# Kernel optimization log

Hardware: AMD Instinct MI355X
Metric: run time of the kernel (lower is better)

The kernel has to match this reference:

```python
import jax, jax.numpy as jnp
import numpy as np

B, L, DIM = 8, 512, 8          # batch, seq len, raw channels (value dim D = 2*DIM = 16)
ET, HID, H = 128, 128, 2       # embed_time, hidden_size, num_heads
MAXLEN = 512
NEG = -1e9


def setup_inputs() -> dict:
    key = jax.random.key(0)
    ks = jax.random.split(key, 40)
    def n(i, shape, s=0.05):
        return jax.random.normal(ks[i], shape, jnp.float32) * s
    vals = jax.random.normal(ks[0], (B, L, DIM), jnp.float32)
    msk = (jax.random.uniform(ks[1], (B, L, DIM)) > 0.2).astype(jnp.float32)
    x = jnp.concatenate([vals, msk], -1)                      # (B, L, 2*DIM)
    time_steps = jax.random.uniform(ks[2], (B, L), jnp.float32)
    return {
        'x': x, 'time_steps': time_steps,
        # learned time embedding: Linear(1, ET-1) periodic + Linear(1,1)
        'w_per': n(3, (1, ET - 1)), 'b_per': n(4, (ET - 1,)),
        'w_lin': n(5, (1, 1)), 'b_lin': n(6, (1,)),
        # MultiTimeAttention projections
        'Wq_t': n(7, (ET, ET)), 'bq_t': n(8, (ET,)),
        'Wk_t': n(9, (ET, ET)), 'bk_t': n(10, (ET,)),
        'Wo_t': n(11, (2 * DIM * H, HID)), 'bo_t': n(12, (HID,)),
        'pos_emb': n(13, (MAXLEN + 1, HID)), 'cls_emb': n(14, (1, HID)),
        # transformer block (BERT-style post-LN encoder layer, d_ff=HID)
        'tWq': n(15, (HID, HID)), 'tbq': n(16, (HID,)),
        'tWk': n(17, (HID, HID)), 'tbk': n(18, (HID,)),
        'tWv': n(19, (HID, HID)), 'tbv': n(20, (HID,)),
        'tWo': n(21, (HID, HID)), 'tbo': n(22, (HID,)),
        'ln1_g': jnp.ones((HID,), jnp.float32), 'ln1_b': jnp.zeros((HID,), jnp.float32),
        'fW1': n(23, (HID, HID)), 'fb1': n(24, (HID,)),
        'fW2': n(25, (HID, HID)), 'fb2': n(26, (HID,)),
        'ln2_g': jnp.ones((HID,), jnp.float32), 'ln2_b': jnp.zeros((HID,), jnp.float32),
        # BertPooler
        'pW': n(27, (HID, HID)), 'pb': n(28, (HID,)),
    }


def _time_emb(tt, w_per, b_per, w_lin, b_lin):
    tt = tt[..., None]                                        # (B, L, 1)
    return jnp.concatenate([tt @ w_lin + b_lin, jnp.sin(tt @ w_per + b_per)], -1)


def _ln(x, g, b, eps=1e-5):
    m = x.mean(-1, keepdims=True)
    v = ((x - m) ** 2).mean(-1, keepdims=True)
    return (x - m) / jnp.sqrt(v + eps) * g + b


def _mta(q_emb, k_emb, value, mask, Wq, bq, Wk, bk, Wo, bo):
    # MultiTimeAttention: scores broadcast to value-channel axis, softmax over keys
    D = value.shape[-1]
    dk = ET // H
    def split(e, W, b):
        p = e @ W + b
        return p.reshape(e.shape[0], -1, H, dk).transpose(0, 2, 1, 3)
    q = split(q_emb, Wq, bq)                                  # (Bq, H, Lq, dk)
    k = split(k_emb, Wk, bk)                                  # (B,  H, Lk, dk)
    scores = jnp.matmul(q, k.swapaxes(-1, -2)) / jnp.sqrt(jnp.float32(dk))  # (B,H,Lq,Lk)
    s5 = jnp.where(mask[:, None, None, :, :] == 0, NEG, scores[..., None])  # (B,H,Lq,Lk,D)
    p = jax.nn.softmax(s5, axis=-2)
    out = jnp.einsum('bhqkd,bkd->bhqd', p, value)             # (B, H, Lq, D)
    Bv = value.shape[0]
    out = out.transpose(0, 2, 1, 3).reshape(Bv, -1, H * D)
    return out @ Wo + bo


def _tblock(x, tWq, tbq, tWk, tbk, tWv, tbv, tWo, tbo, ln1_g, ln1_b,
            fW1, fb1, fW2, fb2, ln2_g, ln2_b):
    Bq, Lq, _ = x.shape
    dk = HID // H
    def heads(W, b):
        return (x @ W + b).reshape(Bq, Lq, H, dk).transpose(0, 2, 1, 3)
    q, k, v = heads(tWq, tbq), heads(tWk, tbk), heads(tWv, tbv)
    a = jax.nn.softmax(jnp.matmul(q, k.swapaxes(-1, -2)) / jnp.sqrt(jnp.float32(dk)), -1)
    o = jnp.matmul(a, v).transpose(0, 2, 1, 3).reshape(Bq, Lq, HID) @ tWo + tbo
    x = _ln(x + o, ln1_g, ln1_b)
    f = jax.nn.relu(x @ fW1 + fb1) @ fW2 + fb2
    return _ln(x + f, ln2_g, ln2_b)


def reference(x, time_steps, w_per, b_per, w_lin, b_lin,
              Wq_t, bq_t, Wk_t, bk_t, Wo_t, bo_t, pos_emb, cls_emb,
              tWq, tbq, tWk, tbk, tWv, tbv, tWo, tbo, ln1_g, ln1_b,
              fW1, fb1, fW2, fb2, ln2_g, ln2_b, pW, pb):
    Bx = x.shape[0]
    mask_half = x[:, :, DIM:]
    mask = jnp.concatenate([mask_half, mask_half], -1)        # (B, L, 2*DIM)
    key_e = _time_emb(time_steps, w_per, b_per, w_lin, b_lin)
    tq_e = _time_emb(time_steps, w_per, b_per, w_lin, b_lin)  # query_time_steps=None -> same
    cls_t = jnp.linspace(0.0, 1.0, 128, dtype=jnp.float32)[None]
    cls_q_e = _time_emb(cls_t, w_per, b_per, w_lin, b_lin)    # (1, 128, ET)
    cls_out = _mta(cls_q_e, key_e, x, mask, Wq_t, bq_t, Wk_t, bk_t, Wo_t, bo_t)
    out = _mta(tq_e, key_e, x, mask, Wq_t, bq_t, Wk_t, bk_t, Wo_t, bo_t)
    tb = (tWq, tbq, tWk, tbk, tWv, tbv, tWo, tbo, ln1_g, ln1_b,
          fW1, fb1, fW2, fb2, ln2_g, ln2_b)
    cls_repr = jnp.broadcast_to(cls_emb[None, :, :], (Bx, 1, HID))
    # encode(cls_out, is_pooling=True), pooling='bert': no pos emb, take token 0
    h = _tblock(jnp.concatenate([cls_repr, cls_out], 1), *tb)
    cls_pooling = jnp.tanh(h[:, 0] @ pW + pb)                 # (B, HID)
    # encode(out, is_pooling=False) [pretrain path]: pos emb + transformer, drop CLS
    h2 = jnp.concatenate([cls_repr, out], 1)                  # (B, L+1, HID)
    h2 = h2 + pos_emb[:h2.shape[1]][None]
    h2 = _tblock(h2, *tb)
    last_hidden_state = h2[:, 1:]                             # (B, L, HID)
    return cls_pooling, last_hidden_state
```

## Files before the change

### kernel.cpp

```cpp
#include <hip/hip_runtime.h>
#include <hip/hip_bf16.h>
#include <math.h>


static constexpr int NM_ = 8 * 513;
static constexpr int NC_ = 8 * 129;
static constexpr int NT_ = NM_ + NC_;
static constexpr int VTS_ = 5248;

using bf = __hip_bfloat16;
typedef __attribute__((ext_vector_type(8))) short bf16x8;
typedef __attribute__((ext_vector_type(4))) short bf16x4;
typedef __attribute__((ext_vector_type(4))) float floatx4;
typedef __attribute__((ext_vector_type(8))) unsigned short ushortx8;

__device__ __forceinline__ float wave_reduce_sum(float v) {
    #pragma unroll
    for (int off = 32; off >= 1; off >>= 1) v += __shfl_xor(v, off);
    return v;
}
__device__ __forceinline__ float wave_reduce_max(float v) {
    #pragma unroll
    for (int off = 32; off >= 1; off >>= 1) v = fmaxf(v, __shfl_xor(v, off));
    return v;
}
__device__ __forceinline__ float u2f(unsigned short u) {
    return __uint_as_float(((unsigned)u) << 16);
}
__device__ __forceinline__ unsigned short f2u(float f) {
    unsigned u = __float_as_uint(f);
    return (unsigned short)((u + 0x7FFF + ((u >> 16) & 1)) >> 16);
}
__device__ __forceinline__ bf16x8 join8(bf16x4 lo, bf16x4 hi) {
    return __builtin_shufflevector(lo, hi, 0, 1, 2, 3, 4, 5, 6, 7);
}
__device__ __forceinline__ float rdin(const void* p, int i, int flag) {
    return flag ? u2f(((const unsigned short*)p)[i]) : ((const float*)p)[i];
}

struct PrepAll {
    const void* src[32]; int n[32]; int dstoff[32];
    int cstart[32]; int cnum[32];
    int ncv;
    const void* wsrc[8]; unsigned short* wdst[8]; float wscale[8];
    const void* ts; const void* w_per; const void* b_per;
    const void* w_lin; const void* b_lin;
    unsigned short* key_e16;
    unsigned short* btg;
    const void* xsrc;
    unsigned short* vt;
    const unsigned short* det;
};
__global__ void prep_all_kernel(PrepAll a, float* dst) {
    int flag = (a.det[0] == 0x3F80u) ? 1 : 0;
    int blk = blockIdx.x, tid = threadIdx.x;
    if (blk < a.ncv) {
        int which = -1, bi = 0;
        #pragma unroll
        for (int i = 0; i < 32; ++i)
            if (blk >= a.cstart[i] && blk < a.cstart[i] + a.cnum[i]) { which = i; bi = blk - a.cstart[i]; }
        if (which < 0) return;
        int i = bi * 256 + tid;
        if (i < a.n[which]) dst[a.dstoff[which] + i] = rdin(a.src[which], i, flag);
    } else if (blk < a.ncv + 512) {
        int p = blk - a.ncv;
        int m = p >> 6;
        int idx = (p & 63) * 256 + tid;
        int c = idx >> 9;
        int l = (idx >> 3) & 63;
        int j = idx & 7;
        int k = (c >> 3) * 32 + (l >> 4) * 8 + j;
        int n = (c & 7) * 16 + (l & 15);
        a.wdst[m][idx] = f2u(rdin(a.wsrc[m], k * 128 + n, flag) * a.wscale[m]);
    } else if (blk < a.ncv + 512 + 2112) {
        int p = blk - a.ncv - 512;
        int row = p * 2 + (tid >> 7), j = tid & 127;
        float t = (row < 4096) ? rdin(a.ts, row, flag)
                               : (float)(row - 4096) * (1.0f / 127.0f);
        float v;
        if (j == 0) v = t * rdin(a.w_lin, 0, flag) + rdin(a.b_lin, 0, flag);
        else        v = sinf(t * rdin(a.w_per, j - 1, flag) + rdin(a.b_per, j - 1, flag));
        a.key_e16[row * 128 + j] = f2u(v);
    } else if (blk < a.ncv + 512 + 2112 + 32) {
        int p = blk - a.ncv - 512 - 2112;
        int e0 = (p * 256 + tid) * 8;
        int b = e0 >> 13;
        int c = (e0 >> 9) & 15;
        int k0 = e0 & 511;
        unsigned short out[8];
        #pragma unroll
        for (int j = 0; j < 8; ++j) {
            int k = k0 + j;
            float m = rdin(a.xsrc, (b * 512 + k) * 16 + 8 + (c & 7), flag);
            float val = (c < 8) ? rdin(a.xsrc, (b * 512 + k) * 16 + c, flag) * m : m;
            out[j] = f2u(val);
        }
        *(ushortx8*)(a.btg + e0) = *(ushortx8*)out;
    } else {
        int p = blk - a.ncv - 512 - 2112 - 32;
        int idx = p * 256 + tid;
        int n = idx / 14, c8 = idx - n * 14;
        ushortx8 z = {0, 0, 0, 0, 0, 0, 0, 0};
        *(ushortx8*)(a.vt + (size_t)n * VTS_ + 5136 + c8 * 8) = z;
    }
}

struct GemmM {
    const void* A[3]; const unsigned short* W[3]; const float* bias[3];
    unsigned short* C[3];
    int M[3]; float bscale[3];
};
__global__ void __launch_bounds__(256)
gemm_mfma_kernel(GemmM p) {
    int y = blockIdx.y;
    const unsigned short* Wsw = p.W[y];
    const float* bias = p.bias[y];
    unsigned short* C = p.C[y];
    int M = p.M[y];
    float bscale = p.bscale[y];
    int m0 = blockIdx.x * 16;
    if (m0 >= M) return;
    int tid = threadIdx.x;
    int wv = tid >> 6, lane = tid & 63;
    int am = lane & 15, aq = lane >> 4;
    const unsigned short* A = (const unsigned short*)p.A[y];
    const unsigned short* Arow = A + (size_t)(m0 + am) * 128;
    floatx4 acc0 = {0.f, 0.f, 0.f, 0.f}, acc1 = acc0;
    #pragma unroll
    for (int ks = 0; ks < 4; ++ks) {
        bf16x8 af = *(const bf16x8*)(Arow + ks * 32 + aq * 8);
        const unsigned short* base = Wsw + ((size_t)ks * 8 + 2 * wv) * 512 + lane * 8;
        bf16x8 b0 = *(const bf16x8*)(base);
        bf16x8 b1 = *(const bf16x8*)(base + 512);
        acc0 = __builtin_amdgcn_mfma_f32_16x16x32_bf16(af, b0, acc0, 0, 0, 0);
        acc1 = __builtin_amdgcn_mfma_f32_16x16x32_bf16(af, b1, acc1, 0, 0, 0);
    }
    int col = lane & 15, rowb = (lane >> 4) * 4;
    #pragma unroll
    for (int t = 0; t < 2; ++t) {
        floatx4 acc = t ? acc1 : acc0;
        int n = wv * 32 + t * 16 + col;
        float bv = bias[n] * bscale;
        #pragma unroll
        for (int rg = 0; rg < 4; ++rg)
            C[(size_t)(m0 + rowb + rg) * 128 + n] = f2u(acc[rg] + bv);
    }
}

__global__ void __launch_bounds__(256)
mta_att_kernel(const unsigned short* qp_cls, const unsigned short* qp_main,
               const unsigned short* kp, const unsigned short* btg,
               float* att_cls, float* att_mn) {
    int is_cls = (blockIdx.x >= 32);
    int qt = is_cls ? (blockIdx.x - 32) : blockIdx.x;
    int h = blockIdx.y, b = blockIdx.z;
    int tid = threadIdx.x, lane = tid & 63, wv = tid >> 6;
    __shared__ unsigned short sp[16][520];
    __shared__ float red[1024 + 256];
    int q0 = qt * 16;
    int m = lane & 15, g = lane >> 4;

    const unsigned short* qrow = is_cls ? (qp_cls + (size_t)(q0 + m) * 128 + h * 64)
                                        : (qp_main + (size_t)(b * 512 + q0 + m) * 128 + h * 64);
    bf16x8 qf0 = *(const bf16x8*)(qrow + g * 8);
    bf16x8 qf1 = *(const bf16x8*)(qrow + 32 + g * 8);

    const unsigned short* kbase = kp + ((size_t)b * 512) * 128 + h * 64;
    #pragma unroll
    for (int kt = 0; kt < 8; ++kt) {
        int colk = kt * 64 + wv * 16 + m;
        const unsigned short* kb = kbase + (size_t)colk * 128;
        bf16x8 b0 = *(const bf16x8*)(kb + g * 8);
        bf16x8 b1 = *(const bf16x8*)(kb + 32 + g * 8);
        floatx4 acc = {0.f, 0.f, 0.f, 0.f};
        acc = __builtin_amdgcn_mfma_f32_16x16x32_bf16(qf0, b0, acc, 0, 0, 0);
        acc = __builtin_amdgcn_mfma_f32_16x16x32_bf16(qf1, b1, acc, 0, 0, 0);
        #pragma unroll
        for (int rg = 0; rg < 4; ++rg) sp[g * 4 + rg][colk] = f2u(acc[rg]);
    }
    __syncthreads();

    for (int rr = wv; rr < 16; rr += 4) {
        float mx = -1e30f;
        for (int k = lane; k < 512; k += 64) mx = fmaxf(mx, u2f(sp[rr][k]));
        mx = wave_reduce_max(mx);
        for (int k = lane; k < 512; k += 64) sp[rr][k] = f2u(expf(u2f(sp[rr][k]) - mx));
    }
    __syncthreads();

    floatx4 macc = {0.f, 0.f, 0.f, 0.f};
    {
        const unsigned short* bbase = btg + ((size_t)(b * 16 + m)) * 512 + g * 8;
        #pragma unroll
        for (int cc = 0; cc < 4; ++cc) {
            int koff = (wv + cc * 4) * 32;
            bf16x8 af = *(const bf16x8*)&sp[m][koff + g * 8];
            bf16x8 bfv = *(const bf16x8*)(bbase + koff);
            macc = __builtin_amdgcn_mfma_f32_16x16x32_bf16(af, bfv, macc, 0, 0, 0);
        }
    }
    float* redC = red;
    float* Cfull = red + 1024;
    #pragma unroll
    for (int rg = 0; rg < 4; ++rg) redC[tid * 4 + rg] = macc[rg];
    __syncthreads();
    {
        int l = tid >> 2, rg = tid & 3;
        float s = redC[l * 4 + rg] + redC[(64 + l) * 4 + rg]
                + redC[(128 + l) * 4 + rg] + redC[(192 + l) * 4 + rg];
        int row = (l >> 4) * 4 + rg, c = l & 15;
        Cfull[row * 16 + c] = s;
    }
    __syncthreads();
    if (tid < 128) {
        int r = tid >> 3, c = tid & 7;
        float num = Cfull[r * 16 + c];
        float den = Cfull[r * 16 + 8 + c];
        int row = q0 + r;
        float* dst = is_cls ? (att_cls + (size_t)(b * 128 + row) * 32)
                            : (att_mn + (size_t)(b * 512 + row) * 32);
        dst[h * 16 + c] = num / den;
        dst[h * 16 + 8 + c] = 1.0f;
    }
}

__global__ void __launch_bounds__(256)
mta_qkv_kernel(const float* att, const float* Wo, const float* bo,
               const float* cls_emb, const float* pos, float* xin,
               const unsigned short* Wq, const unsigned short* Wk, const unsigned short* Wv,
               const float* bq, const float* bk, const float* bv_,
               unsigned short* outq, unsigned short* outk, unsigned short* vT) {
    int m0 = blockIdx.x * 16;
    __shared__ float As32[16][36];
    __shared__ unsigned short As[16][136];
    int tid = threadIdx.x;
    int r = tid >> 4, g = tid & 15, c0 = g * 8;

    int R = m0 + r;
    int srow, prow;
    if (R < NM_) {
        int b = R / 513, rr = R - b * 513;
        srow = (rr == 0) ? -1 : 1024 + b * 512 + (rr - 1);
        prow = rr;
    } else {
        int mc = R - NM_;
        int b = mc / 129, rr = mc - b * 129;
        srow = (rr == 0) ? -1 : b * 128 + (rr - 1);
        prow = -1;
    }
    if (g < 2 && srow >= 0) {
        const float* src = att + (size_t)srow * 32 + g * 16;
        *(float4*)&As32[r][g * 16]      = *(const float4*)(src);
        *(float4*)&As32[r][g * 16 + 4]  = *(const float4*)(src + 4);
        *(float4*)&As32[r][g * 16 + 8]  = *(const float4*)(src + 8);
        *(float4*)&As32[r][g * 16 + 12] = *(const float4*)(src + 12);
    }
    __syncthreads();

    float acc[8];
    if (srow < 0) {
        #pragma unroll
        for (int j = 0; j < 8; ++j) acc[j] = cls_emb[c0 + j];
    } else {
        #pragma unroll
        for (int j = 0; j < 8; ++j) acc[j] = bo[c0 + j];
        #pragma unroll 8
        for (int k = 0; k < 32; ++k) {
            float a = As32[r][k];
            const float4 w0 = *(const float4*)(Wo + (size_t)k * 128 + c0);
            const float4 w1 = *(const float4*)(Wo + (size_t)k * 128 + c0 + 4);
            acc[0] = fmaf(a, w0.x, acc[0]); acc[1] = fmaf(a, w0.y, acc[1]);
            acc[2] = fmaf(a, w0.z, acc[2]); acc[3] = fmaf(a, w0.w, acc[3]);
            acc[4] = fmaf(a, w1.x, acc[4]); acc[5] = fmaf(a, w1.y, acc[5]);
            acc[6] = fmaf(a, w1.z, acc[6]); acc[7] = fmaf(a, w1.w, acc[7]);
        }
    }
    if (prow >= 0) {
        const float* pr = pos + (size_t)prow * 128 + c0;
        float4 p0 = *(const float4*)(pr);
        float4 p1 = *(const float4*)(pr + 4);
        acc[0] += p0.x; acc[1] += p0.y; acc[2] += p0.z; acc[3] += p0.w;
        acc[4] += p1.x; acc[5] += p1.y; acc[6] += p1.z; acc[7] += p1.w;
    }
    *(float4*)(xin + (size_t)R * 128 + c0) = make_float4(acc[0], acc[1], acc[2], acc[3]);
    *(float4*)(xin + (size_t)R * 128 + c0 + 4) = make_float4(acc[4], acc[5], acc[6], acc[7]);
    *(ushort4*)&As[r][c0] = make_ushort4(f2u(acc[0]), f2u(acc[1]), f2u(acc[2]), f2u(acc[3]));
    *(ushort4*)&As[r][c0 + 4] = make_ushort4(f2u(acc[4]), f2u(acc[5]), f2u(acc[6]), f2u(acc[7]));
    __syncthreads();

    int wv = tid >> 6, lane = tid & 63;
    int am = lane & 15, aq = lane >> 4;
    int col = lane & 15, rowb = (lane >> 4) * 4;
    const unsigned short* Ws[3] = {Wq, Wk, Wv};
    const float* bs[3] = {bq, bk, bv_};
    float bsc[3] = {0.125f, 1.f, 1.f};
    unsigned short* Cs[2] = {outq, outk};
    #pragma unroll
    for (int y = 0; y < 3; ++y) {
        floatx4 acc0 = {0.f, 0.f, 0.f, 0.f}, acc1 = acc0;
        #pragma unroll
        for (int ks = 0; ks < 4; ++ks) {
            bf16x8 af = *(bf16x8*)&As[am][ks * 32 + aq * 8];
            const unsigned short* base = Ws[y] + ((size_t)ks * 8 + 2 * wv) * 512 + lane * 8;
            bf16x8 b0 = *(const bf16x8*)(base);
            bf16x8 b1 = *(const bf16x8*)(base + 512);
            acc0 = __builtin_amdgcn_mfma_f32_16x16x32_bf16(af, b0, acc0, 0, 0, 0);
            acc1 = __builtin_amdgcn_mfma_f32_16x16x32_bf16(af, b1, acc1, 0, 0, 0);
        }
        #pragma unroll
        for (int t = 0; t < 2; ++t) {
            floatx4 a2 = t ? acc1 : acc0;
            int n = wv * 32 + t * 16 + col;
            float bvv = bs[y][n] * bsc[y];
            #pragma unroll
            for (int rg = 0; rg < 4; ++rg) {
                unsigned short val = f2u(a2[rg] + bvv);
                if (y < 2) Cs[y][(size_t)(m0 + rowb + rg) * 128 + n] = val;
                else       vT[(size_t)n * VTS_ + (m0 + rowb + rg)] = val;
            }
        }
    }
}

__global__ void __launch_bounds__(256)
tb_att_kernel(const unsigned short* qp, const unsigned short* kp,
              const unsigned short* vT, unsigned short* outp) {
    int is_cls = (blockIdx.x >= 33);
    int qt = is_cls ? blockIdx.x - 33 : blockIdx.x;
    int h = blockIdx.y, b = blockIdx.z;
    int Lq = is_cls ? 129 : 513;
    int base = is_cls ? (4104 + b * 129) : (b * 513);
    int nkt = is_cls ? 3 : 9;
    int tid = threadIdx.x, lane = tid & 63, wv = tid >> 6;
    __shared__ unsigned short sp[16][588];
    __shared__ float rinv[16];
    int q0 = qt * 16;
    int m = lane & 15, g = lane >> 4;

    int qr = q0 + m; if (qr >= Lq) qr = Lq - 1;
    const unsigned short* qrow = qp + (size_t)(base + qr) * 128 + h * 64;
    bf16x8 qf0 = *(const bf16x8*)(qrow + g * 8);
    bf16x8 qf1 = *(const bf16x8*)(qrow + 32 + g * 8);

    for (int kt = 0; kt < nkt; ++kt) {
        int colk = kt * 64 + wv * 16 + m;
        int krow = (colk < Lq) ? colk : (Lq - 1);
        const unsigned short* kb = kp + (size_t)(base + krow) * 128 + h * 64;
        bf16x8 b0 = *(const bf16x8*)(kb + g * 8);
        bf16x8 b1 = *(const bf16x8*)(kb + 32 + g * 8);
        floatx4 acc = {0.f, 0.f, 0.f, 0.f};
        acc = __builtin_amdgcn_mfma_f32_16x16x32_bf16(qf0, b0, acc, 0, 0, 0);
        acc = __builtin_amdgcn_mfma_f32_16x16x32_bf16(qf1, b1, acc, 0, 0, 0);
        #pragma unroll
        for (int rg = 0; rg < 4; ++rg)
            sp[g * 4 + rg][colk] = f2u((colk < Lq) ? acc[rg] : -1e30f);
    }
    __syncthreads();

    int kend = nkt * 64;
    for (int rr = wv; rr < 16; rr += 4) {
        float mx = -1e30f;
        for (int k = lane; k < kend; k += 64) mx = fmaxf(mx, u2f(sp[rr][k]));
        mx = wave_reduce_max(mx);
        float sum = 0.f;
        for (int k = lane; k < kend; k += 64) {
            float e = expf(u2f(sp[rr][k]) - mx);
            sp[rr][k] = f2u(e);
            sum += e;
        }
        sum = wave_reduce_sum(sum);
        if (lane == 0) rinv[rr] = 1.f / sum;
    }
    __syncthreads();

    floatx4 oacc = {0.f, 0.f, 0.f, 0.f};
    const unsigned short* vbase = vT + (size_t)(h * 64 + wv * 16 + m) * VTS_ + base;
    for (int kt = 0; kt < nkt; ++kt) {
        int k0 = kt * 64;
        #pragma unroll
        for (int c = 0; c < 2; ++c) {
            bf16x4 plo = *(const bf16x4*)&sp[m][k0 + c * 32 + g * 8];
            bf16x4 phi = *(const bf16x4*)&sp[m][k0 + c * 32 + g * 8 + 4];
            bf16x8 vf = *(const bf16x8*)(vbase + k0 + c * 32 + g * 8);
            oacc = __builtin_amdgcn_mfma_f32_16x16x32_bf16(join8(plo, phi), vf, oacc, 0, 0, 0);
        }
    }
    int dcol = wv * 16 + m;
    #pragma unroll
    for (int rg = 0; rg < 4; ++rg) {
        int q = g * 4 + rg;
        int qout = q0 + q;
        if (qout < Lq)
            outp[(size_t)(base + qout) * 128 + h * 64 + dcol] = f2u(oacc[rg] * rinv[q]);
    }
}

__global__ void __launch_bounds__(256)
attnout_ffn_kernel(const unsigned short* A, const unsigned short* Wao, const float* bao,
                   const float* resid, const float* g1, const float* b1ln,
                   const unsigned short* W1, const float* fb1,
                   const unsigned short* W2, const float* fb2,
                   const float* g2, const float* b2ln,
                   const float* pW, const float* pb, float* dout) {
    int m0 = blockIdx.x * 16;
    __shared__ unsigned short As[16][136];
    __shared__ float Xs[16][128];
    __shared__ unsigned short Hs[16][136];
    __shared__ float redS[4][4][4], redQ[4][4][4];
    __shared__ float smean[16], sinv[16];
    __shared__ float x2row[128];
    __shared__ int poolb;
    int tid = threadIdx.x;
    if (tid == 0) poolb = -1;
    {
        int r = tid >> 4, c0 = (tid & 15) * 8;
        *(ushortx8*)&As[r][c0] = *(const ushortx8*)(A + (size_t)(m0 + r) * 128 + c0);
    }
    __syncthreads();

    int wv = tid >> 6, lane = tid & 63;
    int am = lane & 15, aq = lane >> 4;
    int col = lane & 15, g = lane >> 4, rowb = g * 4;

    float ov[2][4];
    {
        floatx4 acc0 = {0.f, 0.f, 0.f, 0.f}, acc1 = acc0;
        #pragma unroll
        for (int ks = 0; ks < 4; ++ks) {
            bf16x8 af = *(bf16x8*)&As[am][ks * 32 + aq * 8];
            const unsigned short* base = Wao + ((size_t)ks * 8 + 2 * wv) * 512 + lane * 8;
            bf16x8 bb0 = *(const bf16x8*)(base);
            bf16x8 bb1 = *(const bf16x8*)(base + 512);
            acc0 = __builtin_amdgcn_mfma_f32_16x16x32_bf16(af, bb0, acc0, 0, 0, 0);
            acc1 = __builtin_amdgcn_mfma_f32_16x16x32_bf16(af, bb1, acc1, 0, 0, 0);
        }
        #pragma unroll
        for (int t = 0; t < 2; ++t) {
            int n = wv * 32 + t * 16 + col;
            float bv = bao[n];
            floatx4 acc = t ? acc1 : acc0;
            #pragma unroll
            for (int rg = 0; rg < 4; ++rg)
                ov[t][rg] = acc[rg] + bv + resid[(size_t)(m0 + rowb + rg) * 128 + n];
        }
    }
    #pragma unroll
    for (int rg = 0; rg < 4; ++rg) {
        float s = ov[0][rg] + ov[1][rg];
        float q = ov[0][rg] * ov[0][rg] + ov[1][rg] * ov[1][rg];
        #pragma unroll
        for (int off = 8; off >= 1; off >>= 1) {
            s += __shfl_xor(s, off);
            q += __shfl_xor(q, off);
        }
        if ((lane & 15) == 0) { redS[wv][g][rg] = s; redQ[wv][g][rg] = q; }
    }
    __syncthreads();
    if (tid < 16) {
        int gg = tid >> 2, rg = tid & 3;
        float s = redS[0][gg][rg] + redS[1][gg][rg] + redS[2][gg][rg] + redS[3][gg][rg];
        float q = redQ[0][gg][rg] + redQ[1][gg][rg] + redQ[2][gg][rg] + redQ[3][gg][rg];
        float mean = s * 0.0078125f;
        float var = q * 0.0078125f - mean * mean;
        smean[tid] = mean;
        sinv[tid] = rsqrtf(var + 1e-5f);
    }
    __syncthreads();
    #pragma unroll
    for (int t = 0; t < 2; ++t) {
        int n = wv * 32 + t * 16 + col;
        float gm = g1[n], bb = b1ln[n];
        #pragma unroll
        for (int rg = 0; rg < 4; ++rg) {
            int row = rowb + rg;
            float val = (ov[t][rg] - smean[row]) * sinv[row] * gm + bb;
            Xs[row][n] = val;
            As[row][n] = f2u(val);
        }
    }
    __syncthreads();

    {
        floatx4 acc0 = {0.f, 0.f, 0.f, 0.f}, acc1 = acc0;
        #pragma unroll
        for (int ks = 0; ks < 4; ++ks) {
            bf16x8 af = *(bf16x8*)&As[am][ks * 32 + aq * 8];
            const unsigned short* base = W1 + ((size_t)ks * 8 + 2 * wv) * 512 + lane * 8;
            bf16x8 bb0 = *(const bf16x8*)(base);
            bf16x8 bb1 = *(const bf16x8*)(base + 512);
            acc0 = __builtin_amdgcn_mfma_f32_16x16x32_bf16(af, bb0, acc0, 0, 0, 0);
            acc1 = __builtin_amdgcn_mfma_f32_16x16x32_bf16(af, bb1, acc1, 0, 0, 0);
        }
        #pragma unroll
        for (int t = 0; t < 2; ++t) {
            int n = wv * 32 + t * 16 + col;
            float bv = fb1[n];
            floatx4 acc = t ? acc1 : acc0;
            #pragma unroll
            for (int rg = 0; rg < 4; ++rg)
                Hs[rowb + rg][n] = f2u(fmaxf(acc[rg] + bv, 0.f));
        }
    }
    __syncthreads();

    floatx4 acc0 = {0.f, 0.f, 0.f, 0.f}, acc1 = acc0;
    #pragma unroll
    for (int ks = 0; ks < 4; ++ks) {
        bf16x8 af = *(bf16x8*)&Hs[am][ks * 32 + aq * 8];
        const unsigned short* base = W2 + ((size_t)ks * 8 + 2 * wv) * 512 + lane * 8;
        bf16x8 bb0 = *(const bf16x8*)(base);
        bf16x8 bb1 = *(const bf16x8*)(base + 512);
        acc0 = __builtin_amdgcn_mfma_f32_16x16x32_bf16(af, bb0, acc0, 0, 0, 0);
        acc1 = __builtin_amdgcn_mfma_f32_16x16x32_bf16(af, bb1, acc1, 0, 0, 0);
    }
    #pragma unroll
    for (int t = 0; t < 2; ++t) {
        int n = wv * 32 + t * 16 + col;
        float bv = fb2[n];
        floatx4 acc = t ? acc1 : acc0;
        #pragma unroll
        for (int rg = 0; rg < 4; ++rg)
            ov[t][rg] = acc[rg] + bv + Xs[rowb + rg][n];
    }
    #pragma unroll
    for (int rg = 0; rg < 4; ++rg) {
        float s = ov[0][rg] + ov[1][rg];
        float q = ov[0][rg] * ov[0][rg] + ov[1][rg] * ov[1][rg];
        #pragma unroll
        for (int off = 8; off >= 1; off >>= 1) {
            s += __shfl_xor(s, off);
            q += __shfl_xor(q, off);
        }
        if ((lane & 15) == 0) { redS[wv][g][rg] = s; redQ[wv][g][rg] = q; }
    }
    __syncthreads();
    if (tid < 16) {
        int gg = tid >> 2, rg = tid & 3;
        float s = redS[0][gg][rg] + redS[1][gg][rg] + redS[2][gg][rg] + redS[3][gg][rg];
        float q = redQ[0][gg][rg] + redQ[1][gg][rg] + redQ[2][gg][rg] + redQ[3][gg][rg];
        float mean = s * 0.0078125f;
        float var = q * 0.0078125f - mean * mean;
        smean[tid] = mean;
        sinv[tid] = rsqrtf(var + 1e-5f);
    }
    __syncthreads();
    #pragma unroll
    for (int t = 0; t < 2; ++t) {
        int n = wv * 32 + t * 16 + col;
        float gm = g2[n], bb = b2ln[n];
        #pragma unroll
        for (int rg = 0; rg < 4; ++rg) {
            int row = rowb + rg;
            int m = m0 + row;
            float val = (ov[t][rg] - smean[row]) * sinv[row] * gm + bb;
            if (m < NM_) {
                int b = m / 513, r = m - b * 513;
                if (r >= 1)
                    dout[1024 + (size_t)b * 65536 + (size_t)(r - 1) * 128 + n] = val;
            } else {
                int mc = m - NM_;
                int b = mc / 129, r = mc - b * 129;
                if (r == 0) {
                    x2row[n] = val;
                    if (n == 0) poolb = b;
                }
            }
        }
    }
    __syncthreads();
    if (poolb >= 0 && tid < 128) {
        float acc = pb[tid];
        for (int k = 0; k < 128; ++k) acc = fmaf(x2row[k], pW[(size_t)k * 128 + tid], acc);
        dout[(size_t)poolb * 128 + tid] = tanhf(acc);
    }
}

extern "C" void kernel_launch(void* const* d_in, const int* in_sizes, int n_in,
                              void* d_out, int out_size, void* d_ws, size_t ws_size,
                              hipStream_t stream) {
    float* w = (float*)d_ws;
    size_t off = 0;
    auto alloc = [&](size_t n) {
        float* p = w + off;
        off += (n + 3) & ~(size_t)3;
        return p;
    };
    auto allocU = [&](size_t n) { return (unsigned short*)alloc((n + 1) / 2); };

    PrepAll pa{};
    int nn = n_in < 32 ? n_in : 32;
    float* fin[32];
    const int needconv[32] = {0,0,0,0,0,0, 0,1, 0,1, 1,1, 1,1, 0,1, 0,1, 0,1,
                              0,1, 1,1, 0,1, 0,1, 1,1, 1,1};
    int ncv = 0;
    for (int i = 0; i < nn; ++i) {
        pa.src[i] = d_in[i];
        pa.n[i] = in_sizes[i];
        fin[i] = alloc(in_sizes[i]);
        pa.dstoff[i] = (int)(fin[i] - w);
        if (needconv[i]) {
            int nb = (in_sizes[i] + 255) / 256;
            pa.cstart[i] = ncv;
            pa.cnum[i] = nb;
            ncv += nb;
        } else { pa.cstart[i] = -1; pa.cnum[i] = 0; }
    }
    for (int i = nn; i < 32; ++i) {
        pa.src[i] = nullptr; pa.n[i] = 0; pa.dstoff[i] = 0;
        pa.cstart[i] = -1; pa.cnum[i] = 0;
    }
    pa.ncv = ncv;

    const float* bq_t    = fin[7];
    const float* bk_t    = fin[9];
    const float* Wo_t    = fin[10]; const float* bo_t = fin[11];
    const float* pos_emb = fin[12]; const float* cls_emb = fin[13];
    const float* tbq = fin[15]; const float* tbk = fin[17]; const float* tbv = fin[19];
    const float* tbo = fin[21];
    const float* ln1_g = fin[22]; const float* ln1_b = fin[23];
    const float* fb1 = fin[25]; const float* fb2 = fin[27];
    const float* ln2_g = fin[28]; const float* ln2_b = fin[29];
    const float* pW = fin[30]; const float* pb = fin[31];

    const int widx[8] = {8, 6, 14, 16, 18, 20, 24, 26};
    unsigned short* wsw[8];
    for (int i = 0; i < 8; ++i) {
        wsw[i] = allocU(16384);
        pa.wsrc[i] = d_in[widx[i]];
        pa.wdst[i] = wsw[i];
        pa.wscale[i] = (i == 1 || i == 2) ? 0.125f : 1.0f;
    }
    pa.ts = d_in[1]; pa.w_per = d_in[2]; pa.b_per = d_in[3];
    pa.w_lin = d_in[4]; pa.b_lin = d_in[5];
    pa.xsrc = d_in[0];
    pa.det = (const unsigned short*)d_in[22];

    unsigned short* key_e16 = allocU(4224 * 128);
    unsigned short* cls_e16 = key_e16 + 4096 * 128;
    pa.key_e16 = key_e16;
    unsigned short* btg = allocU(8 * 16 * 512);
    pa.btg = btg;

    unsigned short* qp_main16 = allocU(4096 * 128);
    unsigned short* kp_main16 = allocU(4096 * 128);
    unsigned short* qp_cls16  = allocU(128 * 128);
    float* att_all = alloc(5120 * 32);
    float* att_cls = att_all;
    float* att_mn  = att_all + 1024 * 32;
    float* xin     = alloc((size_t)NT_ * 128);
    unsigned short* tbq16 = allocU((size_t)NT_ * 128);
    unsigned short* tbk16 = allocU((size_t)NT_ * 128);
    unsigned short* vT    = allocU((size_t)128 * VTS_);
    unsigned short* tba16 = allocU((size_t)NT_ * 128);
    pa.vt = vT;
    (void)ws_size;

    float* outf = (float*)d_out;

    prep_all_kernel<<<ncv + 512 + 2112 + 32 + 7, 256, 0, stream>>>(pa, w);

    {
        GemmM p{};
        p.A[0] = key_e16; p.W[0] = wsw[0]; p.bias[0] = bk_t; p.C[0] = kp_main16;
        p.M[0] = 4096; p.bscale[0] = 1.f;
        p.A[1] = key_e16; p.W[1] = wsw[1]; p.bias[1] = bq_t; p.C[1] = qp_main16;
        p.M[1] = 4096; p.bscale[1] = 0.125f;
        p.A[2] = cls_e16; p.W[2] = wsw[1]; p.bias[2] = bq_t; p.C[2] = qp_cls16;
        p.M[2] = 128; p.bscale[2] = 0.125f;
        gemm_mfma_kernel<<<dim3(256, 3), 256, 0, stream>>>(p);
    }

    mta_att_kernel<<<dim3(40, 2, 8), 256, 0, stream>>>(qp_cls16, qp_main16, kp_main16,
                                                       btg, att_cls, att_mn);

    mta_qkv_kernel<<<321, 256, 0, stream>>>(att_all, Wo_t, bo_t, cls_emb, pos_emb, xin,
                                            wsw[2], wsw[3], wsw[4], tbq, tbk, tbv,
                                            tbq16, tbk16, vT);

    tb_att_kernel<<<dim3(42, 2, 8), 256, 0, stream>>>(tbq16, tbk16, vT, tba16);

    attnout_ffn_kernel<<<321, 256, 0, stream>>>(tba16, wsw[5], tbo, xin, ln1_g, ln1_b,
                                                wsw[6], fb1, wsw[7], fb2, ln2_g, ln2_b,
                                                pW, pb, outf);
}
```

Before: 188.2 us.

## Fuse all pipeline stages into one cooperative persistent kernel with grid syncs

Replaces the six separate kernel launches with a single cooperative kernel that runs every stage as a grid-stride loop over virtual blocks, separated by grid-wide barriers, with shared memory held in a union across stages. Each stage body is pulled out into a device function so the old multi-launch path stays as a fallback when cooperative launch is unavailable. The aim is to remove per-launch overhead and the idle gaps between short kernels. In exchange it adds grid-barrier cost, caps the grid at what fits resident, and pays host-side occupancy and attribute queries on every call.

After: 429.6 us. +128.3%, slower.

```diff
diff --git a/kernel.cpp b/kernel.cpp
--- a/kernel.cpp
+++ b/kernel.cpp
@@ -1,6 +1,9 @@
 #include <hip/hip_runtime.h>
 #include <hip/hip_bf16.h>
+#include <hip/hip_cooperative_groups.h>
 #include <math.h>
+
+namespace cg = cooperative_groups;
 
 
 static constexpr int NM_ = 8 * 513;
@@ -37,6 +40,16 @@
 __device__ __forceinline__ float rdin(const void* p, int i, int flag) {
     return flag ? u2f(((const unsigned short*)p)[i]) : ((const float*)p)[i];
 }
+
+struct MaS { unsigned short sp[16][520]; float red[1280]; };
+struct MqS { float As32[16][36]; unsigned short As[16][136]; };
+struct TbS { unsigned short sp[16][588]; float rinv[16]; };
+struct AoS {
+    unsigned short As[16][136]; float Xs[16][128]; unsigned short Hs[16][136];
+    float redS[4][4][4], redQ[4][4][4], smean[16], sinv[16], x2row[128];
+    int poolb;
+};
+union SMem { MaS ma; MqS mq; TbS tb; AoS ao; };
 
 struct PrepAll {
     const void* src[32]; int n[32]; int dstoff[32];
@@ -51,17 +64,18 @@
     unsigned short* vt;
     const unsigned short* det;
 };
-__global__ void prep_all_kernel(PrepAll a, float* dst) {
-    int flag = (a.det[0] == 0x3F80u) ? 1 : 0;
-    int blk = blockIdx.x, tid = threadIdx.x;
+
+__device__ __forceinline__ void prep_body(const PrepAll& a, float* dst, int blk,
+                                          int tid, int flag) {
     if (blk < a.ncv) {
         int which = -1, bi = 0;
         #pragma unroll
         for (int i = 0; i < 32; ++i)
             if (blk >= a.cstart[i] && blk < a.cstart[i] + a.cnum[i]) { which = i; bi = blk - a.cstart[i]; }
-        if (which < 0) return;
-        int i = bi * 256 + tid;
-        if (i < a.n[which]) dst[a.dstoff[which] + i] = rdin(a.src[which], i, flag);
+        if (which >= 0) {
+            int i = bi * 256 + tid;
+            if (i < a.n[which]) dst[a.dstoff[which] + i] = rdin(a.src[which], i, flag);
+        }
     } else if (blk < a.ncv + 512) {
         int p = blk - a.ncv;
         int m = p >> 6;
@@ -99,10 +113,17 @@
     } else {
         int p = blk - a.ncv - 512 - 2112 - 32;
         int idx = p * 256 + tid;
-        int n = idx / 14, c8 = idx - n * 14;
-        ushortx8 z = {0, 0, 0, 0, 0, 0, 0, 0};
-        *(ushortx8*)(a.vt + (size_t)n * VTS_ + 5136 + c8 * 8) = z;
-    }
+        if (idx < 128 * 14) {
+            int n = idx / 14, c8 = idx - n * 14;
+            ushortx8 z = {0, 0, 0, 0, 0, 0, 0, 0};
+            *(ushortx8*)(a.vt + (size_t)n * VTS_ + 5136 + c8 * 8) = z;
+        }
+    }
+}
+
+__global__ void prep_all_kernel(PrepAll a, float* dst) {
+    int flag = (a.det[0] == 0x3F80u) ? 1 : 0;
+    prep_body(a, dst, blockIdx.x, threadIdx.x, flag);
 }
 
 struct GemmM {
@@ -110,20 +131,12 @@
     unsigned short* C[3];
     int M[3]; float bscale[3];
 };
-__global__ void __launch_bounds__(256)
-gemm_mfma_kernel(GemmM p) {
-    int y = blockIdx.y;
-    const unsigned short* Wsw = p.W[y];
-    const float* bias = p.bias[y];
-    unsigned short* C = p.C[y];
-    int M = p.M[y];
-    float bscale = p.bscale[y];
-    int m0 = blockIdx.x * 16;
-    if (m0 >= M) return;
-    int tid = threadIdx.x;
+
+__device__ __forceinline__ void gemm_body(const unsigned short* A, const unsigned short* Wsw,
+                                          const float* bias, unsigned short* C,
+                                          float bscale, int m0, int tid) {
     int wv = tid >> 6, lane = tid & 63;
     int am = lane & 15, aq = lane >> 4;
-    const unsigned short* A = (const unsigned short*)p.A[y];
     const unsigned short* Arow = A + (size_t)(m0 + am) * 128;
     floatx4 acc0 = {0.f, 0.f, 0.f, 0.f}, acc1 = acc0;
     #pragma unroll
@@ -148,15 +161,22 @@
 }
 
 __global__ void __launch_bounds__(256)
-mta_att_kernel(const unsigned short* qp_cls, const unsigned short* qp_main,
-               const unsigned short* kp, const unsigned short* btg,
-               float* att_cls, float* att_mn) {
-    int is_cls = (blockIdx.x >= 32);
-    int qt = is_cls ? (blockIdx.x - 32) : blockIdx.x;
-    int h = blockIdx.y, b = blockIdx.z;
-    int tid = threadIdx.x, lane = tid & 63, wv = tid >> 6;
-    __shared__ unsigned short sp[16][520];
-    __shared__ float red[1024 + 256];
+gemm_mfma_kernel(GemmM p) {
+    int y = blockIdx.y;
+    int m0 = blockIdx.x * 16;
+    if (m0 >= p.M[y]) return;
+    gemm_body((const unsigned short*)p.A[y], p.W[y], p.bias[y], p.C[y], p.bscale[y],
+              m0, threadIdx.x);
+}
+
+__device__ __forceinline__ void mta_att_body(
+    const unsigned short* qp_cls, const unsigned short* qp_main,
+    const unsigned short* kp, const unsigned short* btg,
+    float* att_cls, float* att_mn,
+    int is_cls, int qt, int h, int b, int tid, MaS* S)
+{
+    __syncthreads();
+    int lane = tid & 63, wv = tid >> 6;
     int q0 = qt * 16;
     int m = lane & 15, g = lane >> 4;
 
@@ -176,15 +196,15 @@
         acc = __builtin_amdgcn_mfma_f32_16x16x32_bf16(qf0, b0, acc, 0, 0, 0);
         acc = __builtin_amdgcn_mfma_f32_16x16x32_bf16(qf1, b1, acc, 0, 0, 0);
         #pragma unroll
-        for (int rg = 0; rg < 4; ++rg) sp[g * 4 + rg][colk] = f2u(acc[rg]);
+        for (int rg = 0; rg < 4; ++rg) S->sp[g * 4 + rg][colk] = f2u(acc[rg]);
     }
     __syncthreads();
 
     for (int rr = wv; rr < 16; rr += 4) {
         float mx = -1e30f;
-        for (int k = lane; k < 512; k += 64) mx = fmaxf(mx, u2f(sp[rr][k]));
+        for (int k = lane; k < 512; k += 64) mx = fmaxf(mx, u2f(S->sp[rr][k]));
         mx = wave_reduce_max(mx);
-        for (int k = lane; k < 512; k += 64) sp[rr][k] = f2u(expf(u2f(sp[rr][k]) - mx));
+        for (int k = lane; k < 512; k += 64) S->sp[rr][k] = f2u(expf(u2f(S->sp[rr][k]) - mx));
     }
     __syncthreads();
 
@@ -194,13 +214,13 @@
         #pragma unroll
         for (int cc = 0; cc < 4; ++cc) {
             int koff = (wv + cc * 4) * 32;
-            bf16x8 af = *(const bf16x8*)&sp[m][koff + g * 8];
+            bf16x8 af = *(const bf16x8*)&S->sp[m][koff + g * 8];
             bf16x8 bfv = *(const bf16x8*)(bbase + koff);
             macc = __builtin_amdgcn_mfma_f32_16x16x32_bf16(af, bfv, macc, 0, 0, 0);
         }
     }
-    float* redC = red;
-    float* Cfull = red + 1024;
+    float* redC = S->red;
+    float* Cfull = S->red + 1024;
     #pragma unroll
     for (int rg = 0; rg < 4; ++rg) redC[tid * 4 + rg] = macc[rg];
     __syncthreads();
@@ -225,15 +245,25 @@
 }
 
 __global__ void __launch_bounds__(256)
-mta_qkv_kernel(const float* att, const float* Wo, const float* bo,
-               const float* cls_emb, const float* pos, float* xin,
-               const unsigned short* Wq, const unsigned short* Wk, const unsigned short* Wv,
-               const float* bq, const float* bk, const float* bv_,
-               unsigned short* outq, unsigned short* outk, unsigned short* vT) {
-    int m0 = blockIdx.x * 16;
-    __shared__ float As32[16][36];
-    __shared__ unsigned short As[16][136];
-    int tid = threadIdx.x;
+mta_att_kernel(const unsigned short* qp_cls, const unsigned short* qp_main,
+               const unsigned short* kp, const unsigned short* btg,
+               float* att_cls, float* att_mn) {
+    __shared__ MaS S;
+    int xx = blockIdx.x;
+    mta_att_body(qp_cls, qp_main, kp, btg, att_cls, att_mn,
+                 xx >= 32, (xx >= 32) ? xx - 32 : xx, blockIdx.y, blockIdx.z,
+                 threadIdx.x, &S);
+}
+
+__device__ __forceinline__ void mta_qkv_body(
+    const float* att, const float* Wo, const float* bo,
+    const float* cls_emb, const float* pos, float* xin,
+    const unsigned short* Wq, const unsigned short* Wk, const unsigned short* Wv,
+    const float* bq, const float* bk, const float* bv_,
+    unsigned short* outq, unsigned short* outk, unsigned short* vT,
+    int m0, int tid, MqS* S)
+{
+    __syncthreads();
     int r = tid >> 4, g = tid & 15, c0 = g * 8;
 
     int R = m0 + r;
@@ -250,10 +280,10 @@
     }
     if (g < 2 && srow >= 0) {
         const float* src = att + (size_t)srow * 32 + g * 16;
-        *(float4*)&As32[r][g * 16]      = *(const float4*)(src);
-        *(float4*)&As32[r][g * 16 + 4]  = *(const float4*)(src + 4);
-        *(float4*)&As32[r][g * 16 + 8]  = *(const float4*)(src + 8);
-        *(float4*)&As32[r][g * 16 + 12] = *(const float4*)(src + 12);
+        *(float4*)&S->As32[r][g * 16]      = *(const float4*)(src);
+        *(float4*)&S->As32[r][g * 16 + 4]  = *(const float4*)(src + 4);
+        *(float4*)&S->As32[r][g * 16 + 8]  = *(const float4*)(src + 8);
+        *(float4*)&S->As32[r][g * 16 + 12] = *(const float4*)(src + 12);
     }
     __syncthreads();
 
@@ -266,7 +296,7 @@
         for (int j = 0; j < 8; ++j) acc[j] = bo[c0 + j];
         #pragma unroll 8
         for (int k = 0; k < 32; ++k) {
-            float a = As32[r][k];
+            float a = S->As32[r][k];
             const float4 w0 = *(const float4*)(Wo + (size_t)k * 128 + c0);
             const float4 w1 = *(const float4*)(Wo + (size_t)k * 128 + c0 + 4);
             acc[0] = fmaf(a, w0.x, acc[0]); acc[1] = fmaf(a, w0.y, acc[1]);
@@ -284,8 +314,8 @@
     }
     *(float4*)(xin + (size_t)R * 128 + c0) = make_float4(acc[0], acc[1], acc[2], acc[3]);
     *(float4*)(xin + (size_t)R * 128 + c0 + 4) = make_float4(acc[4], acc[5], acc[6], acc[7]);
-    *(ushort4*)&As[r][c0] = make_ushort4(f2u(acc[0]), f2u(acc[1]), f2u(acc[2]), f2u(acc[3]));
-    *(ushort4*)&As[r][c0 + 4] = make_ushort4(f2u(acc[4]), f2u(acc[5]), f2u(acc[6]), f2u(acc[7]));
+    *(ushort4*)&S->As[r][c0] = make_ushort4(f2u(acc[0]), f2u(acc[1]), f2u(acc[2]), f2u(acc[3]));
+    *(ushort4*)&S->As[r][c0 + 4] = make_ushort4(f2u(acc[4]), f2u(acc[5]), f2u(acc[6]), f2u(acc[7]));
     __syncthreads();
 
     int wv = tid >> 6, lane = tid & 63;
@@ -300,7 +330,7 @@
         floatx4 acc0 = {0.f, 0.f, 0.f, 0.f}, acc1 = acc0;
         #pragma unroll
         for (int ks = 0; ks < 4; ++ks) {
-            bf16x8 af = *(bf16x8*)&As[am][ks * 32 + aq * 8];
+            bf16x8 af = *(bf16x8*)&S->As[am][ks * 32 + aq * 8];
             const unsigned short* base = Ws[y] + ((size_t)ks * 8 + 2 * wv) * 512 + lane * 8;
             bf16x8 b0 = *(const bf16x8*)(base);
             bf16x8 b1 = *(const bf16x8*)(base + 512);
@@ -323,17 +353,26 @@
 }
 
 __global__ void __launch_bounds__(256)
-tb_att_kernel(const unsigned short* qp, const unsigned short* kp,
-              const unsigned short* vT, unsigned short* outp) {
-    int is_cls = (blockIdx.x >= 33);
-    int qt = is_cls ? blockIdx.x - 33 : blockIdx.x;
-    int h = blockIdx.y, b = blockIdx.z;
+mta_qkv_kernel(const float* att, const float* Wo, const float* bo,
+               const float* cls_emb, const float* pos, float* xin,
+               const unsigned short* Wq, const unsigned short* Wk, const unsigned short* Wv,
+               const float* bq, const float* bk, const float* bv_,
+               unsigned short* outq, unsigned short* outk, unsigned short* vT) {
+    __shared__ MqS S;
+    mta_qkv_body(att, Wo, bo, cls_emb, pos, xin, Wq, Wk, Wv, bq, bk, bv_,
+                 outq, outk, vT, blockIdx.x * 16, threadIdx.x, &S);
+}
+
+__device__ __forceinline__ void tb_att_body(
+    const unsigned short* qp, const unsigned short* kp,
+    const unsigned short* vT, unsigned short* outp,
+    int is_cls, int qt, int h, int b, int tid, TbS* S)
+{
+    __syncthreads();
     int Lq = is_cls ? 129 : 513;
     int base = is_cls ? (4104 + b * 129) : (b * 513);
     int nkt = is_cls ? 3 : 9;
-    int tid = threadIdx.x, lane = tid & 63, wv = tid >> 6;
-    __shared__ unsigned short sp[16][588];
-    __shared__ float rinv[16];
+    int lane = tid & 63, wv = tid >> 6;
     int q0 = qt * 16;
     int m = lane & 15, g = lane >> 4;
 
@@ -353,23 +392,23 @@
         acc = __builtin_amdgcn_mfma_f32_16x16x32_bf16(qf1, b1, acc, 0, 0, 0);
         #pragma unroll
         for (int rg = 0; rg < 4; ++rg)
-            sp[g * 4 + rg][colk] = f2u((colk < Lq) ? acc[rg] : -1e30f);
+            S->sp[g * 4 + rg][colk] = f2u((colk < Lq) ? acc[rg] : -1e30f);
     }
     __syncthreads();
 
     int kend = nkt * 64;
     for (int rr = wv; rr < 16; rr += 4) {
         float mx = -1e30f;
-        for (int k = lane; k < kend; k += 64) mx = fmaxf(mx, u2f(sp[rr][k]));
+        for (int k = lane; k < kend; k += 64) mx = fmaxf(mx, u2f(S->sp[rr][k]));
         mx = wave_reduce_max(mx);
         float sum = 0.f;
         for (int k = lane; k < kend; k += 64) {
-            float e = expf(u2f(sp[rr][k]) - mx);
-            sp[rr][k] = f2u(e);
+            float e = expf(u2f(S->sp[rr][k]) - mx);
+            S->sp[rr][k] = f2u(e);
             sum += e;
         }
         sum = wave_reduce_sum(sum);
-        if (lane == 0) rinv[rr] = 1.f / sum;
+        if (lane == 0) S->rinv[rr] = 1.f / sum;
     }
     __syncthreads();
 
@@ -379,8 +418,8 @@
         int k0 = kt * 64;
         #pragma unroll
         for (int c = 0; c < 2; ++c) {
-            bf16x4 plo = *(const bf16x4*)&sp[m][k0 + c * 32 + g * 8];
-            bf16x4 phi = *(const bf16x4*)&sp[m][k0 + c * 32 + g * 8 + 4];
+            bf16x4 plo = *(const bf16x4*)&S->sp[m][k0 + c * 32 + g * 8];
+            bf16x4 phi = *(const bf16x4*)&S->sp[m][k0 + c * 32 + g * 8 + 4];
             bf16x8 vf = *(const bf16x8*)(vbase + k0 + c * 32 + g * 8);
             oacc = __builtin_amdgcn_mfma_f32_16x16x32_bf16(join8(plo, phi), vf, oacc, 0, 0, 0);
         }
@@ -391,7 +430,190 @@
         int q = g * 4 + rg;
         int qout = q0 + q;
         if (qout < Lq)
-            outp[(size_t)(base + qout) * 128 + h * 64 + dcol] = f2u(oacc[rg] * rinv[q]);
+            outp[(size_t)(base + qout) * 128 + h * 64 + dcol] = f2u(oacc[rg] * S->rinv[q]);
+    }
+}
+
+__global__ void __launch_bounds__(256)
+tb_att_kernel(const unsigned short* qp, const unsigned short* kp,
+              const unsigned short* vT, unsigned short* outp) {
+    __shared__ TbS S;
+    int xx = blockIdx.x;
+    tb_att_body(qp, kp, vT, outp, xx >= 33, (xx >= 33) ? xx - 33 : xx,
+                blockIdx.y, blockIdx.z, threadIdx.x, &S);
+}
+
+__device__ __forceinline__ void attnout_body(
+    const unsigned short* A, const unsigned short* Wao, const float* bao,
+    const float* resid, const float* g1, const float* b1ln,
+    const unsigned short* W1, const float* fb1,
+    const unsigned short* W2, const float* fb2,
+    const float* g2, const float* b2ln,
+    const float* pW, const float* pb, float* dout,
+    int m0, int tid, AoS* S)
+{
+    __syncthreads();
+    if (tid == 0) S->poolb = -1;
+    {
+        int r = tid >> 4, c0 = (tid & 15) * 8;
+        *(ushortx8*)&S->As[r][c0] = *(const ushortx8*)(A + (size_t)(m0 + r) * 128 + c0);
+    }
+    __syncthreads();
+
+    int wv = tid >> 6, lane = tid & 63;
+    int am = lane & 15, aq = lane >> 4;
+    int col = lane & 15, g = lane >> 4, rowb = g * 4;
+
+    float ov[2][4];
+    {
+        floatx4 acc0 = {0.f, 0.f, 0.f, 0.f}, acc1 = acc0;
+        #pragma unroll
+        for (int ks = 0; ks < 4; ++ks) {
+            bf16x8 af = *(bf16x8*)&S->As[am][ks * 32 + aq * 8];
+            const unsigned short* base = Wao + ((size_t)ks * 8 + 2 * wv) * 512 + lane * 8;
+            bf16x8 bb0 = *(const bf16x8*)(base);
+            bf16x8 bb1 = *(const bf16x8*)(base + 512);
+            acc0 = __builtin_amdgcn_mfma_f32_16x16x32_bf16(af, bb0, acc0, 0, 0, 0);
+            acc1 = __builtin_amdgcn_mfma_f32_16x16x32_bf16(af, bb1, acc1, 0, 0, 0);
+        }
+        #pragma unroll
+        for (int t = 0; t < 2; ++t) {
+            int n = wv * 32 + t * 16 + col;
+            float bv = bao[n];
+            floatx4 acc = t ? acc1 : acc0;
+            #pragma unroll
+            for (int rg = 0; rg < 4; ++rg)
+                ov[t][rg] = acc[rg] + bv + resid[(size_t)(m0 + rowb + rg) * 128 + n];
+        }
+    }
+    #pragma unroll
+    for (int rg = 0; rg < 4; ++rg) {
+        float s = ov[0][rg] + ov[1][rg];
+        float q = ov[0][rg] * ov[0][rg] + ov[1][rg] * ov[1][rg];
+        #pragma unroll
+        for (int off = 8; off >= 1; off >>= 1) {
+            s += __shfl_xor(s, off);
+            q += __shfl_xor(q, off);
+        }
+        if ((lane & 15) == 0) { S->redS[wv][g][rg] = s; S->redQ[wv][g][rg] = q; }
+    }
+    __syncthreads();
+    if (tid < 16) {
+        int gg = tid >> 2, rg = tid & 3;
+        float s = S->redS[0][gg][rg] + S->redS[1][gg][rg] + S->redS[2][gg][rg] + S->redS[3][gg][rg];
+        float q = S->redQ[0][gg][rg] + S->redQ[1][gg][rg] + S->redQ[2][gg][rg] + S->redQ[3][gg][rg];
+        float mean = s * 0.0078125f;
+        float var = q * 0.0078125f - mean * mean;
+        S->smean[tid] = mean;
+        S->sinv[tid] = rsqrtf(var + 1e-5f);
+    }
+    __syncthreads();
+    #pragma unroll
+    for (int t = 0; t < 2; ++t) {
+        int n = wv * 32 + t * 16 + col;
+        float gm = g1[n], bb = b1ln[n];
+        #pragma unroll
+        for (int rg = 0; rg < 4; ++rg) {
+            int row = rowb + rg;
+            float val = (ov[t][rg] - S->smean[row]) * S->sinv[row] * gm + bb;
+            S->Xs[row][n] = val;
+            S->As[row][n] = f2u(val);
+        }
+    }
+    __syncthreads();
+
+    {
+        floatx4 acc0 = {0.f, 0.f, 0.f, 0.f}, acc1 = acc0;
+        #pragma unroll
+        for (int ks = 0; ks < 4; ++ks) {
+            bf16x8 af = *(bf16x8*)&S->As[am][ks * 32 + aq * 8];
+            const unsigned short* base = W1 + ((size_t)ks * 8 + 2 * wv) * 512 + lane * 8;
+            bf16x8 bb0 = *(const bf16x8*)(base);
+            bf16x8 bb1 = *(const bf16x8*)(base + 512);
+            acc0 = __builtin_amdgcn_mfma_f32_16x16x32_bf16(af, bb0, acc0, 0, 0, 0);
+            acc1 = __builtin_amdgcn_mfma_f32_16x16x32_bf16(af, bb1, acc1, 0, 0, 0);
+        }
+        #pragma unroll
+        for (int t = 0; t < 2; ++t) {
+            int n = wv * 32 + t * 16 + col;
+            float bv = fb1[n];
+            floatx4 acc = t ? acc1 : acc0;
+            #pragma unroll
+            for (int rg = 0; rg < 4; ++rg)
+                S->Hs[rowb + rg][n] = f2u(fmaxf(acc[rg] + bv, 0.f));
+        }
+    }
+    __syncthreads();
+
+    floatx4 acc0 = {0.f, 0.f, 0.f, 0.f}, acc1 = acc0;
+    #pragma unroll
+    for (int ks = 0; ks < 4; ++ks) {
+        bf16x8 af = *(bf16x8*)&S->Hs[am][ks * 32 + aq * 8];
+        const unsigned short* base = W2 + ((size_t)ks * 8 + 2 * wv) * 512 + lane * 8;
+        bf16x8 bb0 = *(const bf16x8*)(base);
+        bf16x8 bb1 = *(const bf16x8*)(base + 512);
+        acc0 = __builtin_amdgcn_mfma_f32_16x16x32_bf16(af, bb0, acc0, 0, 0, 0);
+        acc1 = __builtin_amdgcn_mfma_f32_16x16x32_bf16(af, bb1, acc1, 0, 0, 0);
+    }
+    #pragma unroll
+    for (int t = 0; t < 2; ++t) {
+        int n = wv * 32 + t * 16 + col;
+        float bv = fb2[n];
+        floatx4 acc = t ? acc1 : acc0;
+        #pragma unroll
+        for (int rg = 0; rg < 4; ++rg)
+            ov[t][rg] = acc[rg] + bv + S->Xs[rowb + rg][n];
+    }
+    #pragma unroll
+    for (int rg = 0; rg < 4; ++rg) {
+        float s = ov[0][rg] + ov[1][rg];
+        float q = ov[0][rg] * ov[0][rg] + ov[1][rg] * ov[1][rg];
+        #pragma unroll
+        for (int off = 8; off >= 1; off >>= 1) {
+            s += __shfl_xor(s, off);
+            q += __shfl_xor(q, off);
+        }
+        if ((lane & 15) == 0) { S->redS[wv][g][rg] = s; S->redQ[wv][g][rg] = q; }
+    }
+    __syncthreads();
+    if (tid < 16) {
+        int gg = tid >> 2, rg = tid & 3;
+        float s = S->redS[0][gg][rg] + S->redS[1][gg][rg] + S->redS[2][gg][rg] + S->redS[3][gg][rg];
+        float q = S->redQ[0][gg][rg] + S->redQ[1][gg][rg] + S->redQ[2][gg][rg] + S->redQ[3][gg][rg];
+        float mean = s * 0.0078125f;
+        float var = q * 0.0078125f - mean * mean;
+        S->smean[tid] = mean;
+        S->sinv[tid] = rsqrtf(var + 1e-5f);
+    }
+    __syncthreads();
+    #pragma unroll
+    for (int t = 0; t < 2; ++t) {
+        int n = wv * 32 + t * 16 + col;
+        float gm = g2[n], bb = b2ln[n];
+        #pragma unroll
+        for (int rg = 0; rg < 4; ++rg) {
+            int row = rowb + rg;
+            int mm = m0 + row;
+            float val = (ov[t][rg] - S->smean[row]) * S->sinv[row] * gm + bb;
+            if (mm < NM_) {
+                int b = mm / 513, r = mm - b * 513;
+                if (r >= 1)
+                    dout[1024 + (size_t)b * 65536 + (size_t)(r - 1) * 128 + n] = val;
+            } else {
+                int mc = mm - NM_;
+                int b = mc / 129, r = mc - b * 129;
+                if (r == 0) {
+                    S->x2row[n] = val;
+                    if (n == 0) S->poolb = b;
+                }
+            }
+        }
+    }
+    __syncthreads();
+    if (S->poolb >= 0 && tid < 128) {
+        float acc = pb[tid];
+        for (int k = 0; k < 128; ++k) acc = fmaf(S->x2row[k], pW[(size_t)k * 128 + tid], acc);
+        dout[(size_t)S->poolb * 128 + tid] = tanhf(acc);
     }
 }
 
@@ -402,177 +624,73 @@
                    const unsigned short* W2, const float* fb2,
                    const float* g2, const float* b2ln,
                    const float* pW, const float* pb, float* dout) {
-    int m0 = blockIdx.x * 16;
-    __shared__ unsigned short As[16][136];
-    __shared__ float Xs[16][128];
-    __shared__ unsigned short Hs[16][136];
-    __shared__ float redS[4][4][4], redQ[4][4][4];
-    __shared__ float smean[16], sinv[16];
-    __shared__ float x2row[128];
-    __shared__ int poolb;
+    __shared__ AoS S;
+    attnout_body(A, Wao, bao, resid, g1, b1ln, W1, fb1, W2, fb2, g2, b2ln,
+                 pW, pb, dout, blockIdx.x * 16, threadIdx.x, &S);
+}
+
+struct FusedArgs {
+    PrepAll pa;
+    float* wbase;
+    int prep_nblk;
+    const unsigned short* gA[3]; const unsigned short* gW[3];
+    const float* gBias[3]; unsigned short* gC[3]; float gbs[3];
+    const unsigned short* qp_cls; const unsigned short* qp_main;
+    const unsigned short* kp; const unsigned short* btg;
+    float* att_cls; float* att_mn;
+    const float* att; const float* Wo; const float* bo;
+    const float* cls_emb; const float* pos; float* xin;
+    const unsigned short* Wq; const unsigned short* Wk; const unsigned short* Wv;
+    const float* bq; const float* bk; const float* bv;
+    unsigned short* outq; unsigned short* outk; unsigned short* vT;
+    unsigned short* tba;
+    const unsigned short* Wao; const float* bao;
+    const float* g1; const float* b1ln;
+    const unsigned short* W1; const float* fb1;
+    const unsigned short* W2; const float* fb2;
+    const float* g2; const float* b2ln;
+    const float* pW; const float* pb; float* dout;
+};
+
+__global__ void __launch_bounds__(256, 2)
+fused_kernel(FusedArgs fa) {
+    __shared__ SMem sm;
+    cg::grid_group gg = cg::this_grid();
     int tid = threadIdx.x;
-    if (tid == 0) poolb = -1;
+
     {
-        int r = tid >> 4, c0 = (tid & 15) * 8;
-        *(ushortx8*)&As[r][c0] = *(const ushortx8*)(A + (size_t)(m0 + r) * 128 + c0);
-    }
-    __syncthreads();
-
-    int wv = tid >> 6, lane = tid & 63;
-    int am = lane & 15, aq = lane >> 4;
-    int col = lane & 15, g = lane >> 4, rowb = g * 4;
-
-    float ov[2][4];
-    {
-        floatx4 acc0 = {0.f, 0.f, 0.f, 0.f}, acc1 = acc0;
-        #pragma unroll
-        for (int ks = 0; ks < 4; ++ks) {
-            bf16x8 af = *(bf16x8*)&As[am][ks * 32 + aq * 8];
-            const unsigned short* base = Wao + ((size_t)ks * 8 + 2 * wv) * 512 + lane * 8;
-            bf16x8 bb0 = *(const bf16x8*)(base);
-            bf16x8 bb1 = *(const bf16x8*)(base + 512);
-            acc0 = __builtin_amdgcn_mfma_f32_16x16x32_bf16(af, bb0, acc0, 0, 0, 0);
-            acc1 = __builtin_amdgcn_mfma_f32_16x16x32_bf16(af, bb1, acc1, 0, 0, 0);
-        }
-        #pragma unroll
-        for (int t = 0; t < 2; ++t) {
-            int n = wv * 32 + t * 16 + col;
-            float bv = bao[n];
-            floatx4 acc = t ? acc1 : acc0;
-            #pragma unroll
-            for (int rg = 0; rg < 4; ++rg)
-                ov[t][rg] = acc[rg] + bv + resid[(size_t)(m0 + rowb + rg) * 128 + n];
-        }
-    }
-    #pragma unroll
-    for (int rg = 0; rg < 4; ++rg) {
-        float s = ov[0][rg] + ov[1][rg];
-        float q = ov[0][rg] * ov[0][rg] + ov[1][rg] * ov[1][rg];
-        #pragma unroll
-        for (int off = 8; off >= 1; off >>= 1) {
-            s += __shfl_xor(s, off);
-            q += __shfl_xor(q, off);
-        }
-        if ((lane & 15) == 0) { redS[wv][g][rg] = s; redQ[wv][g][rg] = q; }
-    }
-    __syncthreads();
-    if (tid < 16) {
-        int gg = tid >> 2, rg = tid & 3;
-        float s = redS[0][gg][rg] + redS[1][gg][rg] + redS[2][gg][rg] + redS[3][gg][rg];
-        float q = redQ[0][gg][rg] + redQ[1][gg][rg] + redQ[2][gg][rg] + redQ[3][gg][rg];
-        float mean = s * 0.0078125f;
-        float var = q * 0.0078125f - mean * mean;
-        smean[tid] = mean;
-        sinv[tid] = rsqrtf(var + 1e-5f);
-    }
-    __syncthreads();
-    #pragma unroll
-    for (int t = 0; t < 2; ++t) {
-        int n = wv * 32 + t * 16 + col;
-        float gm = g1[n], bb = b1ln[n];
-        #pragma unroll
-        for (int rg = 0; rg < 4; ++rg) {
-            int row = rowb + rg;
-            float val = (ov[t][rg] - smean[row]) * sinv[row] * gm + bb;
-            Xs[row][n] = val;
-            As[row][n] = f2u(val);
-        }
-    }
-    __syncthreads();
-
-    {
-        floatx4 acc0 = {0.f, 0.f, 0.f, 0.f}, acc1 = acc0;
-        #pragma unroll
-        for (int ks = 0; ks < 4; ++ks) {
-            bf16x8 af = *(bf16x8*)&As[am][ks * 32 + aq * 8];
-            const unsigned short* base = W1 + ((size_t)ks * 8 + 2 * wv) * 512 + lane * 8;
-            bf16x8 bb0 = *(const bf16x8*)(base);
-            bf16x8 bb1 = *(const bf16x8*)(base + 512);
-            acc0 = __builtin_amdgcn_mfma_f32_16x16x32_bf16(af, bb0, acc0, 0, 0, 0);
-            acc1 = __builtin_amdgcn_mfma_f32_16x16x32_bf16(af, bb1, acc1, 0, 0, 0);
-        }
-        #pragma unroll
-        for (int t = 0; t < 2; ++t) {
-            int n = wv * 32 + t * 16 + col;
-            float bv = fb1[n];
-            floatx4 acc = t ? acc1 : acc0;
-            #pragma unroll
-            for (int rg = 0; rg < 4; ++rg)
-                Hs[rowb + rg][n] = f2u(fmaxf(acc[rg] + bv, 0.f));
-        }
-    }
-    __syncthreads();
-
-    floatx4 acc0 = {0.f, 0.f, 0.f, 0.f}, acc1 = acc0;
-    #pragma unroll
-    for (int ks = 0; ks < 4; ++ks) {
-        bf16x8 af = *(bf16x8*)&Hs[am][ks * 32 + aq * 8];
-        const unsigned short* base = W2 + ((size_t)ks * 8 + 2 * wv) * 512 + lane * 8;
-        bf16x8 bb0 = *(const bf16x8*)(base);
-        bf16x8 bb1 = *(const bf16x8*)(base + 512);
-        acc0 = __builtin_amdgcn_mfma_f32_16x16x32_bf16(af, bb0, acc0, 0, 0, 0);
-        acc1 = __builtin_amdgcn_mfma_f32_16x16x32_bf16(af, bb1, acc1, 0, 0, 0);
-    }
-    #pragma unroll
-    for (int t = 0; t < 2; ++t) {
-        int n = wv * 32 + t * 16 + col;
-        float bv = fb2[n];
-        floatx4 acc = t ? acc1 : acc0;
-        #pragma unroll
-        for (int rg = 0; rg < 4; ++rg)
-            ov[t][rg] = acc[rg] + bv + Xs[rowb + rg][n];
-    }
-    #pragma unroll
-    for (int rg = 0; rg < 4; ++rg) {
-        float s = ov[0][rg] + ov[1][rg];
-        float q = ov[0][rg] * ov[0][rg] + ov[1][rg] * ov[1][rg];
-        #pragma unroll
-        for (int off = 8; off >= 1; off >>= 1) {
-            s += __shfl_xor(s, off);
-            q += __shfl_xor(q, off);
-        }
-        if ((lane & 15) == 0) { redS[wv][g][rg] = s; redQ[wv][g][rg] = q; }
-    }
-    __syncthreads();
-    if (tid < 16) {
-        int gg = tid >> 2, rg = tid & 3;
-        float s = redS[0][gg][rg] + redS[1][gg][rg] + redS[2][gg][rg] + redS[3][gg][rg];
-        float q = redQ[0][gg][rg] + redQ[1][gg][rg] + redQ[2][gg][rg] + redQ[3][gg][rg];
-        float mean = s * 0.0078125f;
-        float var = q * 0.0078125f - mean * mean;
-        smean[tid] = mean;
-        sinv[tid] = rsqrtf(var + 1e-5f);
-    }
-    __syncthreads();
-    #pragma unroll
-    for (int t = 0; t < 2; ++t) {
-        int n = wv * 32 + t * 16 + col;
-        float gm = g2[n], bb = b2ln[n];
-        #pragma unroll
-        for (int rg = 0; rg < 4; ++rg) {
-            int row = rowb + rg;
-            int m = m0 + row;
-            float val = (ov[t][rg] - smean[row]) * sinv[row] * gm + bb;
-            if (m < NM_) {
-                int b = m / 513, r = m - b * 513;
-                if (r >= 1)
-                    dout[1024 + (size_t)b * 65536 + (size_t)(r - 1) * 128 + n] = val;
-            } else {
-                int mc = m - NM_;
-                int b = mc / 129, r = mc - b * 129;
-                if (r == 0) {
-                    x2row[n] = val;
-                    if (n == 0) poolb = b;
-                }
-            }
-        }
-    }
-    __syncthreads();
-    if (poolb >= 0 && tid < 128) {
-        float acc = pb[tid];
-        for (int k = 0; k < 128; ++k) acc = fmaf(x2row[k], pW[(size_t)k * 128 + tid], acc);
-        dout[(size_t)poolb * 128 + tid] = tanhf(acc);
-    }
+        int flag = (fa.pa.det[0] == 0x3F80u) ? 1 : 0;
+        for (int blk = blockIdx.x; blk < fa.prep_nblk; blk += gridDim.x)
+            prep_body(fa.pa, fa.wbase, blk, tid, flag);
+    }
+    gg.sync();
+    for (int vb = blockIdx.x; vb < 520; vb += gridDim.x) {
+        int y = (vb < 256) ? 0 : ((vb < 512) ? 1 : 2);
+        int bx = vb - ((y == 0) ? 0 : ((y == 1) ? 256 : 512));
+        gemm_body(fa.gA[y], fa.gW[y], fa.gBias[y], fa.gC[y], fa.gbs[y], bx * 16, tid);
+    }
+    gg.sync();
+    for (int vb = blockIdx.x; vb < 640; vb += gridDim.x) {
+        int xx = vb % 40, h = (vb / 40) & 1, b = vb / 80;
+        mta_att_body(fa.qp_cls, fa.qp_main, fa.kp, fa.btg, fa.att_cls, fa.att_mn,
+                     xx >= 32, (xx >= 32) ? xx - 32 : xx, h, b, tid, &sm.ma);
+    }
+    gg.sync();
+    for (int vb = blockIdx.x; vb < 321; vb += gridDim.x)
+        mta_qkv_body(fa.att, fa.Wo, fa.bo, fa.cls_emb, fa.pos, fa.xin,
+                     fa.Wq, fa.Wk, fa.Wv, fa.bq, fa.bk, fa.bv,
+                     fa.outq, fa.outk, fa.vT, vb * 16, tid, &sm.mq);
+    gg.sync();
+    for (int vb = blockIdx.x; vb < 672; vb += gridDim.x) {
+        int xx = vb % 42, h = (vb / 42) & 1, b = vb / 84;
+        tb_att_body(fa.outq, fa.outk, fa.vT, fa.tba,
+                    xx >= 33, (xx >= 33) ? xx - 33 : xx, h, b, tid, &sm.tb);
+    }
+    gg.sync();
+    for (int vb = blockIdx.x; vb < 321; vb += gridDim.x)
+        attnout_body(fa.tba, fa.Wao, fa.bao, fa.xin, fa.g1, fa.b1ln,
+                     fa.W1, fa.fb1, fa.W2, fa.fb2, fa.g2, fa.b2ln,
+                     fa.pW, fa.pb, fa.dout, vb * 16, tid, &sm.ao);
 }
 
 extern "C" void kernel_launch(void* const* d_in, const int* in_sizes, int n_in,
@@ -656,30 +774,63 @@
     (void)ws_size;
 
     float* outf = (float*)d_out;
-
-    prep_all_kernel<<<ncv + 512 + 2112 + 32 + 7, 256, 0, stream>>>(pa, w);
-
-    {
-        GemmM p{};
-        p.A[0] = key_e16; p.W[0] = wsw[0]; p.bias[0] = bk_t; p.C[0] = kp_main16;
-        p.M[0] = 4096; p.bscale[0] = 1.f;
-        p.A[1] = key_e16; p.W[1] = wsw[1]; p.bias[1] = bq_t; p.C[1] = qp_main16;
-        p.M[1] = 4096; p.bscale[1] = 0.125f;
-        p.A[2] = cls_e16; p.W[2] = wsw[1]; p.bias[2] = bq_t; p.C[2] = qp_cls16;
-        p.M[2] = 128; p.bscale[2] = 0.125f;
-        gemm_mfma_kernel<<<dim3(256, 3), 256, 0, stream>>>(p);
-    }
-
-    mta_att_kernel<<<dim3(40, 2, 8), 256, 0, stream>>>(qp_cls16, qp_main16, kp_main16,
-                                                       btg, att_cls, att_mn);
-
-    mta_qkv_kernel<<<321, 256, 0, stream>>>(att_all, Wo_t, bo_t, cls_emb, pos_emb, xin,
-                                            wsw[2], wsw[3], wsw[4], tbq, tbk, tbv,
-                                            tbq16, tbk16, vT);
-
-    tb_att_kernel<<<dim3(42, 2, 8), 256, 0, stream>>>(tbq16, tbk16, vT, tba16);
-
-    attnout_ffn_kernel<<<321, 256, 0, stream>>>(tba16, wsw[5], tbo, xin, ln1_g, ln1_b,
-                                                wsw[6], fb1, wsw[7], fb2, ln2_g, ln2_b,
-                                                pW, pb, outf);
-}
+    int prep_nblk = ncv + 512 + 2112 + 32 + 7;
+
+    FusedArgs fa{};
+    fa.pa = pa; fa.wbase = w; fa.prep_nblk = prep_nblk;
+    fa.gA[0] = key_e16; fa.gW[0] = wsw[0]; fa.gBias[0] = bk_t; fa.gC[0] = kp_main16; fa.gbs[0] = 1.f;
+    fa.gA[1] = key_e16; fa.gW[1] = wsw[1]; fa.gBias[1] = bq_t; fa.gC[1] = qp_main16; fa.gbs[1] = 0.125f;
+    fa.gA[2] = cls_e16; fa.gW[2] = wsw[1]; fa.gBias[2] = bq_t; fa.gC[2] = qp_cls16;  fa.gbs[2] = 0.125f;
+    fa.qp_cls = qp_cls16; fa.qp_main = qp_main16; fa.kp = kp_main16; fa.btg = btg;
+    fa.att_cls = att_cls; fa.att_mn = att_mn;
+    fa.att = att_all; fa.Wo = Wo_t; fa.bo = bo_t; fa.cls_emb = cls_emb; fa.pos = pos_emb;
+    fa.xin = xin;
+    fa.Wq = wsw[2]; fa.Wk = wsw[3]; fa.Wv = wsw[4];
+    fa.bq = tbq; fa.bk = tbk; fa.bv = tbv;
+    fa.outq = tbq16; fa.outk = tbk16; fa.vT = vT; fa.tba = tba16;
+    fa.Wao = wsw[5]; fa.bao = tbo; fa.g1 = ln1_g; fa.b1ln = ln1_b;
+    fa.W1 = wsw[6]; fa.fb1 = fb1; fa.W2 = wsw[7]; fa.fb2 = fb2;
+    fa.g2 = ln2_g; fa.b2ln = ln2_b; fa.pW = pW; fa.pb = pb; fa.dout = outf;
+
+    bool launched = false;
+    int dev = 0;
+    (void)hipGetDevice(&dev);
+    int coop = 0;
+    (void)hipDeviceGetAttribute(&coop, hipDeviceAttributeCooperativeLaunch, dev);
+    if (coop) {
+        int occ = 0, ncu = 0;
+        (void)hipOccupancyMaxActiveBlocksPerMultiprocessor(&occ, (const void*)fused_kernel, 256, 0);
+        (void)hipDeviceGetAttribute(&ncu, hipDeviceAttributeMultiprocessorCount, dev);
+        int G = occ * ncu;
+        if (G > 672) G = 672;
+        if (G >= 64) {
+            void* params[1] = { (void*)&fa };
+            if (hipLaunchCooperativeKernel((const void*)fused_kernel, dim3(G), dim3(256),
+                                           params, 0, stream) == hipSuccess)
+                launched = true;
+        }
+    }
+
+    if (!launched) {
+        prep_all_kernel<<<prep_nblk, 256, 0, stream>>>(pa, w);
+        {
+            GemmM p{};
+            p.A[0] = key_e16; p.W[0] = wsw[0]; p.bias[0] = bk_t; p.C[0] = kp_main16;
+            p.M[0] = 4096; p.bscale[0] = 1.f;
+            p.A[1] = key_e16; p.W[1] = wsw[1]; p.bias[1] = bq_t; p.C[1] = qp_main16;
+            p.M[1] = 4096; p.bscale[1] = 0.125f;
+            p.A[2] = cls_e16; p.W[2] = wsw[1]; p.bias[2] = bq_t; p.C[2] = qp_cls16;
+            p.M[2] = 128; p.bscale[2] = 0.125f;
+            gemm_mfma_kernel<<<dim3(256, 3), 256, 0, stream>>>(p);
+        }
+        mta_att_kernel<<<dim3(40, 2, 8), 256, 0, stream>>>(qp_cls16, qp_main16, kp_main16,
+                                                           btg, att_cls, att_mn);
+        mta_qkv_kernel<<<321, 256, 0, stream>>>(att_all, Wo_t, bo_t, cls_emb, pos_emb, xin,
+                                                wsw[2], wsw[3], wsw[4], tbq, tbk, tbv,
+                                                tbq16, tbk16, vT);
+        tb_att_kernel<<<dim3(42, 2, 8), 256, 0, stream>>>(tbq16, tbk16, vT, tba16);
+        attnout_ffn_kernel<<<321, 256, 0, stream>>>(tba16, wsw[5], tbo, xin, ln1_g, ln1_b,
+                                                    wsw[6], fb1, wsw[7], fb2, ln2_g, ln2_b,
+                                                    pW, pb, outf);
+    }
+}
```
